# Kernel optimization log

Measured on AMD Instinct MI355X. Metric: run time of the kernel, lower is better.

Reference implementation:

```python
import jax, jax.numpy as jnp
import numpy as np

B, L, D, H, C = 16, 1024, 2048, 512, 2  # batch, doc_len, input_dim, hidden_dim, num_labels


def setup_inputs() -> dict:
    key = jax.random.key(0)
    ks = jax.random.split(key, 8)
    s_ih = 1.0 / np.sqrt(H)
    inp = {
        "x": jax.random.normal(ks[0], (B, L, D), dtype=jnp.float32),
        # PyTorch LSTM params (single layer, gate order i,f,g,o)
        "W_ih": jax.random.uniform(ks[1], (4 * H, D), minval=-s_ih, maxval=s_ih, dtype=jnp.float32),
        "W_hh": jax.random.uniform(ks[2], (4 * H, H), minval=-s_ih, maxval=s_ih, dtype=jnp.float32),
        "b_ih": jax.random.uniform(ks[3], (4 * H,), minval=-s_ih, maxval=s_ih, dtype=jnp.float32),
        "b_hh": jax.random.uniform(ks[4], (4 * H,), minval=-s_ih, maxval=s_ih, dtype=jnp.float32),
        # classifier linear
        "W_lin": jax.random.normal(ks[5], (C, H), dtype=jnp.float32) * 0.02,
        "b_lin": jnp.zeros((C,), dtype=jnp.float32),
        # attention gates, initialized as in the torch module
        "fwd_att": jnp.full((1, H), 0.001, dtype=jnp.float32),
        "bwd_att": jnp.full((1, H), 0.001, dtype=jnp.float32),
    }
    return inp


def _lstm(x, W_ih, W_hh, b_ih, b_hh):
    # x: [B, L, D] -> lstm_out: [B, L, H]
    b = b_ih + b_hh
    xg = jnp.einsum("bld,gd->blg", x, W_ih) + b  # precompute input projection [B,L,4H]

    def step(carry, xg_t):
        h, c = carry
        gates = xg_t + h @ W_hh.T
        i, f, g, o = jnp.split(gates, 4, axis=-1)
        i, f, o = jax.nn.sigmoid(i), jax.nn.sigmoid(f), jax.nn.sigmoid(o)
        g = jnp.tanh(g)
        c = f * c + i * g
        h = o * jnp.tanh(c)
        return (h, c), h

    h0 = jnp.zeros((x.shape[0], W_hh.shape[1]), dtype=x.dtype)
    _, hs = jax.lax.scan(step, (h0, h0), jnp.swapaxes(xg, 0, 1))
    return jnp.swapaxes(hs, 0, 1)  # [B, L, H]


def reference(x, W_ih, W_hh, b_ih, b_hh, W_lin, b_lin, fwd_att, bwd_att):
    lstm_out = _lstm(x, W_ih, W_hh, b_ih, b_hh)  # [B, L, H]
    # per-position gate: argmax of the linear classifier (same for fwd and bwd sums)
    logits = jnp.einsum("blh,ch->blc", lstm_out, W_lin) + b_lin  # [B, L, C]
    g = jnp.argmax(logits, axis=-1).astype(lstm_out.dtype)[..., None]  # [B, L, 1]
    term_f = g * lstm_out * fwd_att  # [B, L, H]
    term_b = g * lstm_out * bwd_att
    # forward_sum[i] = sum_{j<i} term_f[j]  (exclusive prefix sum)
    inc_f = jnp.cumsum(term_f, axis=1)
    cum_f = inc_f - term_f
    # backward_sum[i] = sum_{j>i} term_b[j]  (exclusive suffix sum)
    inc_b = jnp.cumsum(term_b, axis=1)
    cum_b = inc_b[:, -1:, :] - inc_b
    # fused = (lstm_out + cum_f) + (lstm_out + cum_b)
    return 2.0 * lstm_out + cum_f + cum_b
```

## Files before the change

kernel.cpp:

```cpp
#include <hip/hip_runtime.h>
#include <stdint.h>

typedef __bf16 bf16x8_t __attribute__((ext_vector_type(8)));
typedef float  f32x4_t  __attribute__((ext_vector_type(4)));

#define MFMA_BF16(A, Bv, C) __builtin_amdgcn_mfma_f32_16x16x32_bf16((A), (Bv), (C), 0, 0, 0)

static constexpr int BB = 16;
static constexpr int LL = 1024;
static constexpr int DD = 2048;
static constexpr int HH = 512;
static constexpr int GG = 4 * HH;
static constexpr int MM = BB * LL;

static constexpr size_t XBF_OFF   = 0;
static constexpr size_t WIHBF_OFF = XBF_OFF   + (size_t)MM * DD * 2;
static constexpr size_t WHHBF_OFF = WIHBF_OFF + (size_t)GG * DD * 2;
static constexpr size_t XGBF_OFF  = WHHBF_OFF + (size_t)GG * HH * 2;
static constexpr size_t GARR_OFF  = XGBF_OFF  + (size_t)MM * GG * 2;
static constexpr size_t PART_OFF  = GARR_OFF  + (size_t)MM * 4;
static constexpr size_t TBUF_OFF  = PART_OFF  + (size_t)BB * 8 * HH * 4;
static constexpr size_t LBUF_OFF  = TBUF_OFF  + (size_t)2 * BB * HH * 4;
static constexpr size_t WS_NEED   = LBUF_OFF  + (size_t)2 * BB * HH * 4;

__device__ __forceinline__ unsigned short f2bf(float f) {
  union { float f; uint32_t u; } v; v.f = f;
  uint32_t r = v.u + 0x7FFFu + ((v.u >> 16) & 1u);
  return (unsigned short)(r >> 16);
}
__device__ __forceinline__ float bf2f(unsigned short s) {
  union { uint32_t u; float f; } v; v.u = ((uint32_t)s) << 16;
  return v.f;
}
__device__ __forceinline__ float sigmoidf_fast(float x) { return 1.f / (1.f + __expf(-x)); }
__device__ __forceinline__ float tanhf_fast(float x) {
  float ax = fabsf(x);
  float e  = __expf(2.f * ax);
  float t  = 1.f - 2.f / (e + 1.f);
  return copysignf(t, x);
}
__device__ __forceinline__ void async_cp16(const void* g, void* lds) {
  __builtin_amdgcn_global_load_lds((const __attribute__((address_space(1))) uint32_t*)g,
                                   (__attribute__((address_space(3))) uint32_t*)lds, 16, 0, 0);
}

__global__ __launch_bounds__(256) void k_f32_to_bf16(const float* __restrict__ s,
                                                     unsigned short* __restrict__ d, int n4) {
  int i = blockIdx.x * 256 + threadIdx.x;
  int stride = gridDim.x * 256;
  for (; i < n4; i += stride) {
    float4 v = ((const float4*)s)[i];
    ushort4 o;
    o.x = f2bf(v.x); o.y = f2bf(v.y); o.z = f2bf(v.z); o.w = f2bf(v.w);
    ((ushort4*)d)[i] = o;
  }
}

__global__ __launch_bounds__(256) void k_gemm_xg(const unsigned short* __restrict__ A,
                                                 const unsigned short* __restrict__ Bw,
                                                 const float* __restrict__ b_ih,
                                                 const float* __restrict__ b_hh,
                                                 unsigned short* __restrict__ C) {
  __shared__ __align__(16) unsigned short As[128 * 32];
  __shared__ __align__(16) unsigned short Bs[128 * 32];
  const int bid = blockIdx.x;
  const int bn = bid & 15, bm = bid >> 4;
  const int row0 = bm * 128, col0 = bn * 128;
  const int tid = threadIdx.x;
  const int lane = tid & 63, w = tid >> 6;
  const int wr = w >> 1, wc = w & 1;
  const int l15 = lane & 15, l4 = lane >> 4;

  const f32x4_t z4 = {0.f, 0.f, 0.f, 0.f};
  f32x4_t acc[4][4];
#pragma unroll
  for (int mi = 0; mi < 4; ++mi)
#pragma unroll
    for (int ni = 0; ni < 4; ++ni) acc[mi][ni] = z4;

  const unsigned short* ga = A  + (size_t)(row0 + (tid >> 2)) * DD + (tid & 3) * 8;
  const unsigned short* gb = Bw + (size_t)(col0 + (tid >> 2)) * DD + (tid & 3) * 8;
  unsigned short* asw = As + w * 512;
  unsigned short* bsw = Bs + w * 512;

  for (int k0 = 0; k0 < DD; k0 += 32) {
    async_cp16(ga + k0,           asw);
    async_cp16(ga + k0 + 64 * DD, asw + 2048);
    async_cp16(gb + k0,           bsw);
    async_cp16(gb + k0 + 64 * DD, bsw + 2048);
    __syncthreads();
    bf16x8_t af[4], bfr[4];
#pragma unroll
    for (int mi = 0; mi < 4; ++mi)
      af[mi] = *(const bf16x8_t*)(As + (wr * 64 + mi * 16 + l15) * 32 + l4 * 8);
#pragma unroll
    for (int ni = 0; ni < 4; ++ni)
      bfr[ni] = *(const bf16x8_t*)(Bs + (wc * 64 + ni * 16 + l15) * 32 + l4 * 8);
#pragma unroll
    for (int mi = 0; mi < 4; ++mi)
#pragma unroll
      for (int ni = 0; ni < 4; ++ni)
        acc[mi][ni] = MFMA_BF16(af[mi], bfr[ni], acc[mi][ni]);
    __syncthreads();
  }
#pragma unroll
  for (int ni = 0; ni < 4; ++ni) {
    int col = col0 + wc * 64 + ni * 16 + l15;
    float bias = b_ih[col] + b_hh[col];
#pragma unroll
    for (int mi = 0; mi < 4; ++mi) {
      int rowb = row0 + wr * 64 + mi * 16 + l4 * 4;
#pragma unroll
      for (int r = 0; r < 4; ++r)
        C[(size_t)(rowb + r) * GG + col] = f2bf(acc[mi][ni][r] + bias);
    }
  }
}

__global__ __launch_bounds__(256, 1) void k_lstm(const unsigned short* __restrict__ Whh,
                                                 const unsigned short* __restrict__ xg,
                                                 float* __restrict__ h_all,
                                                 unsigned int* tbuf,
                                                 unsigned int* lbuf) {
  const int bid = blockIdx.x;
  const int b  = (bid & 7) + 8 * (bid >> 7);
  const int wg = (bid >> 3) & 15;
  const int tid = threadIdx.x;
  const int lane = tid & 63, w = tid >> 6;
  const int l15 = lane & 15, l4 = lane >> 4;
  const int K0 = wg * 32;

  __shared__ float gl[4][32];
  __shared__ __align__(16) unsigned short h_lds[HH];

  f32x4_t wfr[2][16];
#pragma unroll
  for (int mi = 0; mi < 2; ++mi) {
    const unsigned short* wrow = Whh + (size_t)(w * HH + K0 + mi * 16 + l15) * HH + l4 * 8;
#pragma unroll
    for (int kt = 0; kt < 16; ++kt)
      wfr[mi][kt] = *(const f32x4_t*)(wrow + kt * 32);
  }
#pragma unroll
  for (int mi = 0; mi < 2; ++mi)
#pragma unroll
    for (int kt = 0; kt < 16; ++kt)
      asm volatile("" : "+v"(wfr[mi][kt]));

  float c_reg = 0.f;
  const f32x4_t z4 = {0.f, 0.f, 0.f, 0.f};

  const bool act_lane = (l15 < 8);
  const int r_sel = l15 & 3;
  const int jj = ((l15 >> 2) << 4) + (l4 << 2) + r_sel;
  const unsigned short* xgp = xg + (size_t)(b << 10) * GG + w * HH + K0 + jj;
  float xcur = 0.f;
  if (act_lane) xcur = bf2f(xgp[0]);

  int strikes = 0;

  for (int t = 0; t < LL; ++t) {
    const unsigned long long msk  = 0xFFFF0000FFFF0000ull;
    const unsigned long long tg   = (unsigned long long)(unsigned int)t;
    const unsigned long long expv = (tg << 16) | (tg << 48);
    unsigned long long v = 0;
    bool got = false;

    if (strikes < 8) {
      unsigned long long* lsrc = (unsigned long long*)(lbuf + (((t & 1) * BB + b) << 9)) + tid;
      for (int it = 0; it < 256; ++it) {
        unsigned long long lv;
        asm volatile("global_load_dwordx2 %0, %1, off sc0\n\ts_waitcnt vmcnt(0)"
                     : "=v"(lv) : "v"(lsrc));
        if ((lv & msk) == expv) { v = lv; got = true; break; }
      }
      if (!got) ++strikes;
    }
    if (!got) {
      unsigned long long* src = (unsigned long long*)(tbuf + (((t & 1) * BB + b) << 9)) + tid;
      unsigned int guard = 0;
      for (;;) {
        v = __hip_atomic_load(src, __ATOMIC_RELAXED, __HIP_MEMORY_SCOPE_AGENT);
        if ((v & msk) == expv) break;
        if (++guard > (1u << 20)) break;
      }
    }
    ushort2 hv2; hv2.x = (unsigned short)v; hv2.y = (unsigned short)(v >> 32);
    ((ushort2*)h_lds)[tid] = hv2;
    __syncthreads();

    unsigned short xnx = 0;
    if (act_lane && (t + 1 < LL)) xnx = xgp[(size_t)(t + 1) * GG];

    f32x4_t a0a = z4, a0b = z4, a1a = z4, a1b = z4;
#pragma unroll
    for (int kt = 0; kt < 8; ++kt) {
      bf16x8_t hva = *(const bf16x8_t*)(h_lds + kt * 32 + l4 * 8);
      bf16x8_t hvb = *(const bf16x8_t*)(h_lds + (kt + 8) * 32 + l4 * 8);
      a0a = MFMA_BF16(__builtin_bit_cast(bf16x8_t, wfr[0][kt]),     hva, a0a);
      a1a = MFMA_BF16(__builtin_bit_cast(bf16x8_t, wfr[1][kt]),     hva, a1a);
      a0b = MFMA_BF16(__builtin_bit_cast(bf16x8_t, wfr[0][kt + 8]), hvb, a0b);
      a1b = MFMA_BF16(__builtin_bit_cast(bf16x8_t, wfr[1][kt + 8]), hvb, a1b);
    }

    if (act_lane) {
      f32x4_t s = (l15 >= 4) ? (a1a + a1b) : (a0a + a0b);
      float e01 = (r_sel & 1) ? s[1] : s[0];
      float e23 = (r_sel & 1) ? s[3] : s[2];
      float raw = ((r_sel & 2) ? e23 : e01) + xcur;
      gl[w][jj] = (w == 2) ? tanhf_fast(raw) : sigmoidf_fast(raw);
    }
    __syncthreads();

    if (tid < 32) {
      float gi = gl[0][tid], gf = gl[1][tid], gc = gl[2][tid], go = gl[3][tid];
      c_reg = gf * c_reg + gi * gc;
      float h = go * tanhf_fast(c_reg);
      unsigned int word = ((unsigned int)(t + 1) << 16) | (unsigned int)f2bf(h);
      const int off = ((((t + 1) & 1) * BB + b) << 9) + K0 + tid;
      unsigned int* ldst = lbuf + off;
      asm volatile("global_store_dword %0, %1, off" :: "v"(ldst), "v"(word) : "memory");
      __hip_atomic_store(tbuf + off, word, __ATOMIC_RELAXED, __HIP_MEMORY_SCOPE_AGENT);
      h_all[(size_t)((b << 10) + t) * HH + K0 + tid] = h;
    }

    if (act_lane) xcur = bf2f(xnx);
  }
}

__global__ __launch_bounds__(256) void k_gsel(const float* __restrict__ h, const float* __restrict__ Wlin,
                                              const float* __restrict__ blin, float* __restrict__ g) {
  const int lane = threadIdx.x & 63, w = threadIdx.x >> 6;
  const int idx = blockIdx.x * 4 + w;
  const float4* hp = (const float4*)(h + (size_t)idx * HH + lane * 8);
  const float4* w0 = (const float4*)(Wlin + lane * 8);
  const float4* w1 = (const float4*)(Wlin + HH + lane * 8);
  float4 h0 = hp[0], h1 = hp[1];
  float4 a0 = w0[0], a1 = w0[1], c0 = w1[0], c1 = w1[1];
  float s0 = h0.x*a0.x + h0.y*a0.y + h0.z*a0.z + h0.w*a0.w
           + h1.x*a1.x + h1.y*a1.y + h1.z*a1.z + h1.w*a1.w;
  float s1 = h0.x*c0.x + h0.y*c0.y + h0.z*c0.z + h0.w*c0.w
           + h1.x*c1.x + h1.y*c1.y + h1.z*c1.z + h1.w*c1.w;
#pragma unroll
  for (int off = 32; off > 0; off >>= 1) {
    s0 += __shfl_xor(s0, off);
    s1 += __shfl_xor(s1, off);
  }
  if (lane == 0) g[idx] = (s1 + blin[1] > s0 + blin[0]) ? 1.f : 0.f;
}

__global__ __launch_bounds__(256) void k_scan_a(const float* __restrict__ h, const float* __restrict__ g,
                                                float* __restrict__ part) {
  const int bid = blockIdx.x;
  const int b = bid >> 4, seg = (bid >> 1) & 7, kc = bid & 1;
  const int k = kc * 256 + threadIdx.x;
  __shared__ float gs[128];
  if (threadIdx.x < 128) gs[threadIdx.x] = g[b * LL + seg * 128 + threadIdx.x];
  __syncthreads();
  const float* hp = h + ((size_t)(b * LL + seg * 128)) * HH + k;
  float sum = 0.f;
#pragma unroll 4
  for (int l = 0; l < 128; ++l) sum += gs[l] * hp[(size_t)l * HH];
  part[(b * 8 + seg) * HH + k] = sum;
}

__global__ __launch_bounds__(256) void k_scan_b(float* __restrict__ h, const float* __restrict__ g,
                                                const float* __restrict__ part,
                                                const float* __restrict__ fwd, const float* __restrict__ bwd) {
  const int bid = blockIdx.x;
  const int b = bid >> 4, seg = (bid >> 1) & 7, kc = bid & 1;
  const int k = kc * 256 + threadIdx.x;
  __shared__ float gs[128];
  if (threadIdx.x < 128) gs[threadIdx.x] = g[b * LL + seg * 128 + threadIdx.x];
  __syncthreads();
  float base = 0.f, total = 0.f;
#pragma unroll
  for (int s = 0; s < 8; ++s) {
    float v = part[(b * 8 + s) * HH + k];
    total += v;
    if (s < seg) base += v;
  }
  const float fa = fwd[k], ba = bwd[k];
  float run = base;
  float* hp = h + ((size_t)(b * LL + seg * 128)) * HH + k;
  for (int l = 0; l < 128; ++l) {
    float hv = hp[(size_t)l * HH];
    float term = gs[l] * hv;
    hp[(size_t)l * HH] = 2.f * hv + fa * run + ba * (total - run - term);
    run += term;
  }
}

extern "C" void kernel_launch(void* const* d_in, const int* in_sizes, int n_in,
                              void* d_out, int out_size, void* d_ws, size_t ws_size,
                              hipStream_t stream) {
  if (ws_size < WS_NEED) return;
  const float* x    = (const float*)d_in[0];
  const float* Wih  = (const float*)d_in[1];
  const float* Whh  = (const float*)d_in[2];
  const float* b_ih = (const float*)d_in[3];
  const float* b_hh = (const float*)d_in[4];
  const float* Wlin = (const float*)d_in[5];
  const float* blin = (const float*)d_in[6];
  const float* fwd  = (const float*)d_in[7];
  const float* bwd  = (const float*)d_in[8];
  char* ws = (char*)d_ws;
  unsigned short* xbf   = (unsigned short*)(ws + XBF_OFF);
  unsigned short* wihbf = (unsigned short*)(ws + WIHBF_OFF);
  unsigned short* whhbf = (unsigned short*)(ws + WHHBF_OFF);
  unsigned short* xgbf  = (unsigned short*)(ws + XGBF_OFF);
  float*          garr  = (float*)(ws + GARR_OFF);
  float*          part  = (float*)(ws + PART_OFF);
  unsigned int*   tbuf  = (unsigned int*)(ws + TBUF_OFF);
  unsigned int*   lbuf  = (unsigned int*)(ws + LBUF_OFF);
  float* out = (float*)d_out;

  (void)hipMemsetAsync(ws + TBUF_OFF, 0, (size_t)4 * BB * HH * 4, stream);

  k_f32_to_bf16<<<2048, 256, 0, stream>>>(x,   xbf,   MM * DD / 4);
  k_f32_to_bf16<<<1024, 256, 0, stream>>>(Wih, wihbf, GG * DD / 4);
  k_f32_to_bf16<<<256,  256, 0, stream>>>(Whh, whhbf, GG * HH / 4);
  k_gemm_xg<<<(MM / 128) * (GG / 128), 256, 0, stream>>>(xbf, wihbf, b_ih, b_hh, xgbf);
  k_lstm<<<256, 256, 0, stream>>>(whhbf, xgbf, out, tbuf, lbuf);
  k_gsel<<<MM / 4, 256, 0, stream>>>(out, Wlin, blin, garr);
  k_scan_a<<<256, 256, 0, stream>>>(out, garr, part);
  k_scan_b<<<256, 256, 0, stream>>>(out, garr, part, fwd, bwd);
}
```

Baseline: 1.947 ms.

## Map LSTM batch groups to XCDs at runtime and overlap h polling with gate-update waves

Each block reports its XCC id into a table, and the kernel checks whether the default or a contiguous block-to-(batch, hidden-slice) mapping keeps every batch's 16 workgroups on one XCD. When one does, it polls with non-coherent sc0 loads that stay in the local L2, and falls back to agent-scope atomic loads otherwise. The separate lbuf mirror and its strike heuristic are dropped, and the h exchange buffer is now zeroed inside the kernel rather than by a host memset. Polling moves to waves 0-2 so that wave 3 can produce the next h and store it. This adds a startup barrier across all blocks through the table, and it relies on every block being co-resident.

```diff
diff --git a/kernel.cpp b/kernel.cpp
--- a/kernel.cpp
+++ b/kernel.cpp
@@ -20,8 +20,8 @@
 static constexpr size_t GARR_OFF  = XGBF_OFF  + (size_t)MM * GG * 2;
 static constexpr size_t PART_OFF  = GARR_OFF  + (size_t)MM * 4;
 static constexpr size_t TBUF_OFF  = PART_OFF  + (size_t)BB * 8 * HH * 4;
-static constexpr size_t LBUF_OFF  = TBUF_OFF  + (size_t)2 * BB * HH * 4;
-static constexpr size_t WS_NEED   = LBUF_OFF  + (size_t)2 * BB * HH * 4;
+static constexpr size_t TABL_OFF  = TBUF_OFF  + (size_t)2 * BB * HH * 4;
+static constexpr size_t WS_NEED   = TABL_OFF  + 256 * 4;
 
 __device__ __forceinline__ unsigned short f2bf(float f) {
   union { float f; uint32_t u; } v; v.f = f;
@@ -121,17 +121,50 @@
                                                  const unsigned short* __restrict__ xg,
                                                  float* __restrict__ h_all,
                                                  unsigned int* tbuf,
-                                                 unsigned int* lbuf) {
+                                                 unsigned int* tabl) {
   const int bid = blockIdx.x;
-  const int b  = (bid & 7) + 8 * (bid >> 7);
-  const int wg = (bid >> 3) & 15;
   const int tid = threadIdx.x;
   const int lane = tid & 63, w = tid >> 6;
   const int l15 = lane & 15, l4 = lane >> 4;
-  const int K0 = wg * 32;
 
   __shared__ float gl[4][32];
   __shared__ __align__(16) unsigned short h_lds[HH];
+  __shared__ unsigned int s_tab[256];
+
+  if (tid == 0) {
+    unsigned int xcd;
+    asm volatile("s_getreg_b32 %0, hwreg(HW_REG_XCC_ID)" : "=s"(xcd));
+    __hip_atomic_store(tabl + bid, (xcd & 0xF) + 1u, __ATOMIC_RELAXED, __HIP_MEMORY_SCOPE_AGENT);
+  }
+  {
+    unsigned int v = 0, guard = 0;
+    for (;;) {
+      v = __hip_atomic_load(tabl + tid, __ATOMIC_RELAXED, __HIP_MEMORY_SCOPE_AGENT);
+      if (v != 0) break;
+      if (++guard > (1u << 18)) break;
+    }
+    s_tab[tid] = v;
+  }
+  __syncthreads();
+  const int rr_ok = __syncthreads_and((int)(s_tab[tid] == s_tab[(tid & 7) | (tid & 128)]));
+  const int ch_ok = __syncthreads_and((int)(s_tab[tid] == s_tab[tid & ~15]));
+  const int sel = rr_ok ? 1 : (ch_ok ? 2 : 0);
+  const bool mode_local = (sel != 0);
+
+  int b, wg;
+  if (sel == 2) { b = bid >> 4;                     wg = bid & 15; }
+  else          { b = (bid & 7) + 8 * (bid >> 7);   wg = (bid >> 3) & 15; }
+  const int K0 = wg * 32;
+
+  if (tid >= 192 && tid < 224) {
+    const int e = tid - 192;
+#pragma unroll
+    for (int p = 0; p < 2; ++p) {
+      unsigned int* dst = tbuf + ((p * BB + b) << 9) + K0 + e;
+      *(volatile unsigned int*)dst = 0u;
+      __hip_atomic_store(dst, 0u, __ATOMIC_RELAXED, __HIP_MEMORY_SCOPE_AGENT);
+    }
+  }
 
   f32x4_t wfr[2][16];
 #pragma unroll
@@ -157,36 +190,42 @@
   float xcur = 0.f;
   if (act_lane) xcur = bf2f(xgp[0]);
 
-  int strikes = 0;
+  const unsigned long long msk = 0xFFFF0000FFFF0000ull;
 
   for (int t = 0; t < LL; ++t) {
-    const unsigned long long msk  = 0xFFFF0000FFFF0000ull;
     const unsigned long long tg   = (unsigned long long)(unsigned int)t;
     const unsigned long long expv = (tg << 16) | (tg << 48);
-    unsigned long long v = 0;
-    bool got = false;
-
-    if (strikes < 8) {
-      unsigned long long* lsrc = (unsigned long long*)(lbuf + (((t & 1) * BB + b) << 9)) + tid;
-      for (int it = 0; it < 256; ++it) {
-        unsigned long long lv;
-        asm volatile("global_load_dwordx2 %0, %1, off sc0\n\ts_waitcnt vmcnt(0)"
-                     : "=v"(lv) : "v"(lsrc));
-        if ((lv & msk) == expv) { v = lv; got = true; break; }
+    unsigned long long* base = (unsigned long long*)(tbuf + (((t & 1) * BB + b) << 9));
+
+    if (tid < 192) {
+      const int nq  = (tid < 64) ? 2 : 1;
+      const int q0  = (tid < 64) ? (tid * 2) : (tid + 64);
+#pragma unroll
+      for (int k = 0; k < 2; ++k) {
+        if (k >= nq) break;
+        unsigned long long* src = base + q0 + k;
+        unsigned long long v = 0;
+        unsigned int guard = 0;
+        bool got = false;
+        for (;;) {
+          if (mode_local) {
+            for (int it = 0; it < 16; ++it) {
+              unsigned long long lv;
+              asm volatile("global_load_dwordx2 %0, %1, off sc0\n\ts_waitcnt vmcnt(0)"
+                           : "=v"(lv) : "v"(src));
+              if ((lv & msk) == expv) { v = lv; got = true; break; }
+            }
+            if (got) break;
+          }
+          v = __hip_atomic_load(src, __ATOMIC_RELAXED, __HIP_MEMORY_SCOPE_AGENT);
+          if ((v & msk) == expv) break;
+          if (++guard > (1u << 18)) break;
+        }
+        const int q = q0 + k;
+        ushort2 hv2; hv2.x = (unsigned short)v; hv2.y = (unsigned short)(v >> 32);
+        ((ushort2*)h_lds)[q] = hv2;
       }
-      if (!got) ++strikes;
-    }
-    if (!got) {
-      unsigned long long* src = (unsigned long long*)(tbuf + (((t & 1) * BB + b) << 9)) + tid;
-      unsigned int guard = 0;
-      for (;;) {
-        v = __hip_atomic_load(src, __ATOMIC_RELAXED, __HIP_MEMORY_SCOPE_AGENT);
-        if ((v & msk) == expv) break;
-        if (++guard > (1u << 20)) break;
-      }
-    }
-    ushort2 hv2; hv2.x = (unsigned short)v; hv2.y = (unsigned short)(v >> 32);
-    ((ushort2*)h_lds)[tid] = hv2;
+    }
     __syncthreads();
 
     unsigned short xnx = 0;
@@ -212,16 +251,16 @@
     }
     __syncthreads();
 
-    if (tid < 32) {
-      float gi = gl[0][tid], gf = gl[1][tid], gc = gl[2][tid], go = gl[3][tid];
+    if (tid >= 192 && tid < 224) {
+      const int e = tid - 192;
+      float gi = gl[0][e], gf = gl[1][e], gc = gl[2][e], go = gl[3][e];
       c_reg = gf * c_reg + gi * gc;
       float h = go * tanhf_fast(c_reg);
       unsigned int word = ((unsigned int)(t + 1) << 16) | (unsigned int)f2bf(h);
-      const int off = ((((t + 1) & 1) * BB + b) << 9) + K0 + tid;
-      unsigned int* ldst = lbuf + off;
-      asm volatile("global_store_dword %0, %1, off" :: "v"(ldst), "v"(word) : "memory");
-      __hip_atomic_store(tbuf + off, word, __ATOMIC_RELAXED, __HIP_MEMORY_SCOPE_AGENT);
-      h_all[(size_t)((b << 10) + t) * HH + K0 + tid] = h;
+      unsigned int* dst = tbuf + ((((t + 1) & 1) * BB + b) << 9) + K0 + e;
+      *(volatile unsigned int*)dst = word;
+      __hip_atomic_store(dst, word, __ATOMIC_RELAXED, __HIP_MEMORY_SCOPE_AGENT);
+      h_all[(size_t)((b << 10) + t) * HH + K0 + e] = h;
     }
 
     if (act_lane) xcur = bf2f(xnx);
@@ -312,16 +351,16 @@
   float*          garr  = (float*)(ws + GARR_OFF);
   float*          part  = (float*)(ws + PART_OFF);
   unsigned int*   tbuf  = (unsigned int*)(ws + TBUF_OFF);
-  unsigned int*   lbuf  = (unsigned int*)(ws + LBUF_OFF);
+  unsigned int*   tabl  = (unsigned int*)(ws + TABL_OFF);
   float* out = (float*)d_out;
 
-  (void)hipMemsetAsync(ws + TBUF_OFF, 0, (size_t)4 * BB * HH * 4, stream);
+  (void)hipMemsetAsync(ws + TABL_OFF, 0, 256 * 4, stream);
 
   k_f32_to_bf16<<<2048, 256, 0, stream>>>(x,   xbf,   MM * DD / 4);
   k_f32_to_bf16<<<1024, 256, 0, stream>>>(Wih, wihbf, GG * DD / 4);
   k_f32_to_bf16<<<256,  256, 0, stream>>>(Whh, whhbf, GG * HH / 4);
   k_gemm_xg<<<(MM / 128) * (GG / 128), 256, 0, stream>>>(xbf, wihbf, b_ih, b_hh, xgbf);
-  k_lstm<<<256, 256, 0, stream>>>(whhbf, xgbf, out, tbuf, lbuf);
+  k_lstm<<<256, 256, 0, stream>>>(whhbf, xgbf, out, tbuf, tabl);
   k_gsel<<<MM / 4, 256, 0, stream>>>(out, Wlin, blin, garr);
   k_scan_a<<<256, 256, 0, stream>>>(out, garr, part);
   k_scan_b<<<256, 256, 0, stream>>>(out, garr, part, fwd, bwd);
```

Result: slower. 3.063 ms (+57.3%).
